# Kernel tuning notes

Hardware: AMD Instinct MI355X
Metric: run time of the kernel (lower is better)

Reference implementation:

```python
import jax, jax.numpy as jnp
import numpy as np

NUM_ENT = 100000   # entity vocabulary
NUM_EDGES = 200000 # KB pairs processed per hop (max_act)
D = 768            # BERT hidden size
NSTEP = 3          # num hops
QLEN = 32          # question length


def setup_inputs() -> dict:
    key = jax.random.key(0)
    ks = jax.random.split(key, 18)
    rn = lambda k, s, scale=1.0: jax.random.normal(k, s, dtype=jnp.float32) * scale
    W = 0.02  # weight init scale
    return {
        "q_emb": rn(ks[0], (1, D)),
        "q_word_h": rn(ks[1], (1, QLEN, D)),
        "desc_emb": rn(ks[2], (NUM_EDGES, D)),
        "step_w1": rn(ks[3], (NSTEP, D, D), W),
        "step_b1": rn(ks[4], (NSTEP, D), W),
        "step_w2": rn(ks[5], (NSTEP, D, D), W),
        "step_b2": rn(ks[6], (NSTEP, D), W),
        "rel_w1": rn(ks[7], (D, 256), W),
        "rel_b1": rn(ks[8], (256,), W),
        "rel_w2": rn(ks[9], (256,), W),
        "rel_b2": rn(ks[10], (1,), W),
        "hop_w1": rn(ks[11], (D, 256), W),
        "hop_b1": rn(ks[12], (256,), W),
        "hop_w2": rn(ks[13], (256, NSTEP), W),
        "hop_b2": rn(ks[14], (NSTEP,), W),
        "kb_pair": jax.random.randint(ks[15], (NUM_EDGES, 2), 0, NUM_ENT, dtype=jnp.int32),
        "topic_ent_idxs": jax.random.randint(ks[16], (4,), 0, NUM_ENT, dtype=jnp.int32),
    }


def reference(q_emb, q_word_h, desc_emb, step_w1, step_b1, step_w2, step_b2,
              rel_w1, rel_b1, rel_w2, rel_b2, hop_w1, hop_b1, hop_w2, hop_b2,
              kb_pair, topic_ent_idxs):
    gelu = lambda x: jax.nn.gelu(x, approximate=False)  # torch nn.GELU default
    # topic entity one-hot init (idx_to_one_hot)
    last_e = jnp.zeros((NUM_ENT,), jnp.float32).at[topic_ent_idxs].set(1.0)
    sub, obj = kb_pair[:, 0], kb_pair[:, 1]
    ent_probs = []
    for t in range(NSTEP):
        # step encoder: Linear -> GELU -> Linear
        cq = gelu(q_emb @ step_w1[t] + step_b1[t]) @ step_w2[t] + step_b2[t]  # [1,D]
        # attention over question words
        q_logits = jnp.einsum('bd,bld->bl', cq, q_word_h)                      # [1,L]
        q_dist = jax.nn.softmax(q_logits, axis=1)
        ctx = jnp.einsum('bl,bld->bd', q_dist, q_word_h) + cq                  # [1,D]
        # relation classifier over edge descriptions: Linear -> GELU -> Linear
        h = gelu((ctx * desc_emb) @ rel_w1 + rel_b1)                           # [E,256]
        d_prob = jax.nn.sigmoid(h @ rel_w2 + rel_b2)                           # [E]
        # follow: gather subject scores, scatter-add to objects
        obj_p = last_e[sub] * d_prob
        last_e = jax.ops.segment_sum(obj_p, obj, num_segments=NUM_ENT)
        # clamp-style renormalization (detached divisor)
        z = jax.lax.stop_gradient(jnp.where(last_e > 1.0, last_e, 1.0))
        last_e = last_e / z
        ent_probs.append(last_e)
    hop_res = jnp.stack(ent_probs, 0)                                          # [T,N]
    hop_attn = jax.nn.softmax(gelu(q_emb @ hop_w1 + hop_b1) @ hop_w2 + hop_b2, axis=1)  # [1,T]
    return (hop_attn @ hop_res)[0]                                             # [N]
```

## Files before the change

kernel.cpp:

```cpp
#include <hip/hip_runtime.h>
#include <math.h>

#define NUM_ENT 100000
#define NUM_EDGES 200000
#define DIM 768
#define BM 64
#define KSTEPS 24
#define NC 16
#define DCH 48

typedef float f32x4 __attribute__((ext_vector_type(4)));
typedef __bf16 bf16x8 __attribute__((ext_vector_type(8)));

#define WS_Y1    0
#define WS_CQ    2304
#define WS_HA    4704
#define WS_HOP1  4736
#define WS_CTX   4992
#define WS_B     7424
#define WS_DPROB 302336
#define WS_P1    302336
#define WS_P1H   339200
#define WS_P2    343296
#define WS_E     902336

__device__ __forceinline__ unsigned short f2bf(float f) {
    unsigned int x = __builtin_bit_cast(unsigned int, f);
    x = x + 0x7fffu + ((x >> 16) & 1u);
    return (unsigned short)(x >> 16);
}

__device__ __forceinline__ float gelu_f(float x) {
    float z = 0.70710678118654752f * x;
    float s = fabsf(z);
    float t = 1.f / (1.f + 0.3275911f * s);
    float p = t * (0.254829592f + t * (-0.284496736f + t * (1.421413741f +
              t * (-1.453152027f + t * 1.061405429f))));
    float e = __expf(-s * s);
    float erfa = copysignf(1.f - p * e, z);
    return 0.5f * x * (1.f + erfa);
}

__global__ void k1a(const float* __restrict__ q, const float* __restrict__ sw1,
                    const float* __restrict__ hw1, float* __restrict__ ws) {
    int b = blockIdx.x, tid = threadIdx.x;
    if (b < 48) {
        int t = b >> 4, c = b & 15;
        const float* w = sw1 + (size_t)t * DIM * DIM + (size_t)c * DCH * DIM;
        float a0 = 0.f, a1 = 0.f, a2 = 0.f;
        for (int d = 0; d < DCH; ++d) {
            float qv = q[c * DCH + d];
            const float* wr = w + (size_t)d * DIM;
            a0 += qv * wr[tid]; a1 += qv * wr[tid + 256]; a2 += qv * wr[tid + 512];
        }
        float* p = ws + WS_P1 + (size_t)b * DIM;
        p[tid] = a0; p[tid + 256] = a1; p[tid + 512] = a2;
    } else {
        int c = b - 48;
        const float* w = hw1 + (size_t)c * DCH * 256;
        float a0 = 0.f;
        for (int d = 0; d < DCH; ++d) a0 += q[c * DCH + d] * w[(size_t)d * 256 + tid];
        ws[WS_P1H + c * 256 + tid] = a0;
    }
}

__global__ void k1b(const float* __restrict__ sb1, const float* __restrict__ hb1,
                    float* __restrict__ ws) {
    int o = blockIdx.x * 256 + threadIdx.x;
    if (o < 2304) {
        int t = o / DIM, j = o % DIM;
        float s = sb1[o];
        for (int c = 0; c < NC; ++c) s += ws[WS_P1 + (size_t)(t * 16 + c) * DIM + j];
        ws[WS_Y1 + o] = gelu_f(s);
    } else if (o < 2560) {
        int j = o - 2304;
        float s = hb1[j];
        for (int c = 0; c < NC; ++c) s += ws[WS_P1H + c * 256 + j];
        ws[WS_HOP1 + j] = gelu_f(s);
    }
}

__global__ void k2a(const float* __restrict__ sw2, float* __restrict__ ws) {
    int b = blockIdx.x, tid = threadIdx.x;
    int t = b >> 4, c = b & 15;
    const float* w = sw2 + (size_t)t * DIM * DIM + (size_t)c * DCH * DIM;
    const float* y = ws + WS_Y1 + t * DIM + c * DCH;
    float a0 = 0.f, a1 = 0.f, a2 = 0.f;
    for (int d = 0; d < DCH; ++d) {
        float yv = y[d];
        const float* wr = w + (size_t)d * DIM;
        a0 += yv * wr[tid]; a1 += yv * wr[tid + 256]; a2 += yv * wr[tid + 512];
    }
    float* p = ws + WS_P2 + (size_t)b * DIM;
    p[tid] = a0; p[tid + 256] = a1; p[tid + 512] = a2;
}

__global__ void k2b(const float* __restrict__ sb2, float* __restrict__ ws) {
    int o = blockIdx.x * 256 + threadIdx.x;
    int t = o / DIM, j = o % DIM;
    float s = sb2[o];
    for (int c = 0; c < NC; ++c) s += ws[WS_P2 + (size_t)(t * 16 + c) * DIM + j];
    ws[WS_CQ + o] = s;
}

__global__ void k345(const float* __restrict__ qwh, const float* __restrict__ hw2,
                     const float* __restrict__ hb2, float* __restrict__ ws) {
    __shared__ float qlog[96];
    int tid = threadIdx.x;
    int w = tid >> 6, lane = tid & 63;
    for (int s = 0; s < 6; ++s) {
        int p = w * 6 + s;
        int t = p >> 5, l = p & 31;
        const float* c = ws + WS_CQ + t * DIM;
        const float* qw = qwh + l * DIM;
        float acc = 0.f;
        for (int i = lane; i < DIM; i += 64) acc += c[i] * qw[i];
        for (int m = 32; m; m >>= 1) acc += __shfl_xor(acc, m);
        if (lane == 0) qlog[p] = acc;
    }
    __syncthreads();
    if (tid < 64) {
        for (int t = 0; t < 3; ++t) {
            float v = (lane < 32) ? qlog[t * 32 + lane] : -1e30f;
            float mx = v;
            for (int m = 1; m < 32; m <<= 1) mx = fmaxf(mx, __shfl_xor(mx, m, 32));
            float e = (lane < 32) ? __expf(v - mx) : 0.f;
            float s = e;
            for (int m = 1; m < 32; m <<= 1) s += __shfl_xor(s, m, 32);
            if (lane < 32) qlog[t * 32 + lane] = e / s;
        }
        float lg = 0.f;
        if (lane < 3) {
            for (int s = 0; s < 256; ++s) lg += ws[WS_HOP1 + s] * hw2[s * 3 + lane];
            lg += hb2[lane];
        }
        float l0 = __shfl(lg, 0), l1 = __shfl(lg, 1), l2 = __shfl(lg, 2);
        if (lane == 0) {
            float mx = fmaxf(l0, fmaxf(l1, l2));
            float e0 = __expf(l0 - mx), e1 = __expf(l1 - mx), e2 = __expf(l2 - mx);
            float s = e0 + e1 + e2;
            ws[WS_HA + 0] = e0 / s; ws[WS_HA + 1] = e1 / s; ws[WS_HA + 2] = e2 / s;
        }
    }
    __syncthreads();
    for (int o = tid; o < 2304; o += 1024) {
        int t = o / DIM, d = o % DIM;
        float acc = ws[WS_CQ + o];
        const float* qd = qlog + t * 32;
        for (int l = 0; l < 32; ++l) acc += qd[l] * qwh[l * DIM + d];
        ws[WS_CTX + o] = acc;
    }
}

__global__ void k6_bmat(const float* __restrict__ rw1, float* __restrict__ ws) {
    int g = blockIdx.x * 256 + threadIdx.x;
    int lane = g & 63, f = g >> 6;
    int ks = f / 48, r = f % 48;
    int t = r >> 4, cf = r & 15;
    int k0 = ks * 32 + (lane >> 4) * 8;
    int col = cf * 16 + (lane & 15);
    const float* ctx = ws + WS_CTX + t * DIM;
    union { unsigned short u[8]; bf16x8 v; } pk;
    #pragma unroll
    for (int j = 0; j < 8; ++j) {
        float v = ctx[k0 + j] * rw1[(size_t)(k0 + j) * 256 + col];
        pk.u[j] = f2bf(v);
    }
    *(bf16x8*)((unsigned short*)(ws + WS_B) + (size_t)g * 8) = pk.v;
}

#define MFMA4(A, B0, B1, B2, B3, RF)                                               \
    acc[RF][0] = __builtin_amdgcn_mfma_f32_16x16x32_bf16(A, B0, acc[RF][0], 0,0,0); \
    acc[RF][1] = __builtin_amdgcn_mfma_f32_16x16x32_bf16(A, B1, acc[RF][1], 0,0,0); \
    acc[RF][2] = __builtin_amdgcn_mfma_f32_16x16x32_bf16(A, B2, acc[RF][2], 0,0,0); \
    acc[RF][3] = __builtin_amdgcn_mfma_f32_16x16x32_bf16(A, B3, acc[RF][3], 0,0,0);

#define MSTEP(KS, B0, B1, B2, B3) {                                                \
    const unsigned short* ab = ab0 + (size_t)(KS) * 2048;                          \
    bf16x8 a;                                                                      \
    a = *(const bf16x8*)(ab);          MFMA4(a, B0, B1, B2, B3, 0)                 \
    a = *(const bf16x8*)(ab + 512);    MFMA4(a, B0, B1, B2, B3, 1)                 \
    a = *(const bf16x8*)(ab + 1024);   MFMA4(a, B0, B1, B2, B3, 2)                 \
    a = *(const bf16x8*)(ab + 1536);   MFMA4(a, B0, B1, B2, B3, 3)                 \
}

#define LOADB(N0, N1, N2, N3, KS) {                                                \
    const unsigned short* p = bp0 + (size_t)(KS) * 24576;                          \
    N0 = *(const bf16x8*)(p);        N1 = *(const bf16x8*)(p + 512);               \
    N2 = *(const bf16x8*)(p + 1024); N3 = *(const bf16x8*)(p + 1536);              \
}

__global__ __launch_bounds__(768, 3)
void k7_gemm(const float* __restrict__ desc, const float* __restrict__ rb1,
             const float* __restrict__ rw2, const float* __restrict__ rb2,
             float* __restrict__ ws) {
    extern __shared__ char lds[];
    unsigned short* aLds = (unsigned short*)lds;
    float* part = (float*)(lds + 98304);

    const unsigned short* bmat = (const unsigned short*)(ws + WS_B);
    float* dprob = ws + WS_DPROB;
    int tid = threadIdx.x, blk = blockIdx.x;
    int wid = tid >> 6, lane = tid & 63;
    int t = wid >> 2, cg = wid & 3;
    int fbase = (t << 4) + (cg << 2);

    const unsigned short* bp0 = bmat + ((size_t)fbase << 9) + lane * 8;

    bf16x8 bA0, bA1, bA2, bA3, bB0, bB1, bB2, bB3;
    bf16x8 bC0, bC1, bC2, bC3, bD0, bD1, bD2, bD3;
    LOADB(bA0, bA1, bA2, bA3, 0)
    LOADB(bB0, bB1, bB2, bB3, 1)
    LOADB(bC0, bC1, bC2, bC3, 2)
    LOADB(bD0, bD1, bD2, bD3, 3)

    #pragma unroll
    for (int i = 0; i < 8; ++i) {
        int gf = i * 768 + tid;
        int l = gf & 63, f = gf >> 6;
        int ks = f >> 2, rf = f & 3;
        int row = rf * 16 + (l & 15);
        int kb = ks * 32 + (l >> 4) * 8;
        const float* src = desc + (size_t)(blk * BM + row) * DIM + kb;
        float4 v0 = *(const float4*)src;
        float4 v1 = *(const float4*)(src + 4);
        bf16x8 pk;
        pk[0] = (__bf16)v0.x; pk[1] = (__bf16)v0.y; pk[2] = (__bf16)v0.z; pk[3] = (__bf16)v0.w;
        pk[4] = (__bf16)v1.x; pk[5] = (__bf16)v1.y; pk[6] = (__bf16)v1.z; pk[7] = (__bf16)v1.w;
        *(bf16x8*)(aLds + (size_t)f * 512 + l * 8) = pk;
    }
    __syncthreads();

    f32x4 acc[4][4];
    #pragma unroll
    for (int rf = 0; rf < 4; ++rf)
        #pragma unroll
        for (int i = 0; i < 4; ++i) acc[rf][i] = f32x4{0.f, 0.f, 0.f, 0.f};

    const unsigned short* ab0 = aLds + lane * 8;

    #pragma unroll 1
    for (int it = 0; it < 6; ++it) {
        int ks = it * 4;
        MSTEP(ks,     bA0, bA1, bA2, bA3)
        if (it < 5) LOADB(bA0, bA1, bA2, bA3, ks + 4)
        MSTEP(ks + 1, bB0, bB1, bB2, bB3)
        if (it < 5) LOADB(bB0, bB1, bB2, bB3, ks + 5)
        MSTEP(ks + 2, bC0, bC1, bC2, bC3)
        if (it < 5) LOADB(bC0, bC1, bC2, bC3, ks + 6)
        MSTEP(ks + 3, bD0, bD1, bD2, bD3)
        if (it < 5) LOADB(bD0, bD1, bD2, bD3, ks + 7)
    }

    int col16 = lane & 15, quart = lane >> 4;
    float b1v[4], w2v[4];
    #pragma unroll
    for (int i = 0; i < 4; ++i) {
        int c = cg * 64 + i * 16 + col16;
        b1v[i] = rb1[c]; w2v[i] = rw2[c];
    }
    #pragma unroll
    for (int rf = 0; rf < 4; ++rf) {
        #pragma unroll
        for (int r = 0; r < 4; ++r) {
            float s = 0.f;
            #pragma unroll
            for (int i = 0; i < 4; ++i)
                s += gelu_f(acc[rf][i][r] + b1v[i]) * w2v[i];
            #pragma unroll
            for (int m = 1; m < 16; m <<= 1) s += __shfl_xor(s, m);
            if (col16 == 0) part[wid * 64 + rf * 16 + quart * 4 + r] = s;
        }
    }
    __syncthreads();
    if (tid < 192) {
        int tt = tid >> 6, row = tid & 63;
        float v = part[(tt * 4 + 0) * 64 + row] + part[(tt * 4 + 1) * 64 + row]
                + part[(tt * 4 + 2) * 64 + row] + part[(tt * 4 + 3) * 64 + row] + rb2[0];
        float p = 1.f / (1.f + __expf(-v));
        dprob[(size_t)tt * NUM_EDGES + blk * BM + row] = p;
    }
}

__global__ void kzero(float* __restrict__ ws) {
    int i = blockIdx.x * 256 + threadIdx.x;
    if (i < 3 * NUM_ENT) ws[WS_E + NUM_ENT + i] = 0.f;
}

__global__ void k9_scatter(const int* __restrict__ kb, const int* __restrict__ topics,
                           float* __restrict__ ws, int t) {
    int e = blockIdx.x * 256 + threadIdx.x;
    if (e >= NUM_EDGES) return;
    int sub = kb[2 * e], obj = kb[2 * e + 1];
    float g;
    if (t == 0) {
        g = (sub == topics[0] || sub == topics[1] || sub == topics[2] || sub == topics[3]) ? 1.f : 0.f;
    } else {
        float v = ws[WS_E + (size_t)t * NUM_ENT + sub];
        g = v / fmaxf(v, 1.f);
    }
    float p = g * ws[WS_DPROB + (size_t)t * NUM_EDGES + e];
    if (p != 0.f) atomicAdd(&ws[WS_E + (size_t)(t + 1) * NUM_ENT + obj], p);
}

__global__ void kout(const float* __restrict__ ws, float* __restrict__ out) {
    int i = blockIdx.x * 256 + threadIdx.x;
    if (i >= NUM_ENT) return;
    float v1 = ws[WS_E + 1 * NUM_ENT + i]; v1 /= fmaxf(v1, 1.f);
    float v2 = ws[WS_E + 2 * NUM_ENT + i]; v2 /= fmaxf(v2, 1.f);
    float v3 = ws[WS_E + 3 * NUM_ENT + i]; v3 /= fmaxf(v3, 1.f);
    out[i] = ws[WS_HA + 0] * v1 + ws[WS_HA + 1] * v2 + ws[WS_HA + 2] * v3;
}

extern "C" void kernel_launch(void* const* d_in, const int* in_sizes, int n_in,
                              void* d_out, int out_size, void* d_ws, size_t ws_size,
                              hipStream_t stream) {
    const float* q_emb   = (const float*)d_in[0];
    const float* qwh     = (const float*)d_in[1];
    const float* desc    = (const float*)d_in[2];
    const float* sw1     = (const float*)d_in[3];
    const float* sb1     = (const float*)d_in[4];
    const float* sw2     = (const float*)d_in[5];
    const float* sb2     = (const float*)d_in[6];
    const float* rw1     = (const float*)d_in[7];
    const float* rb1     = (const float*)d_in[8];
    const float* rw2     = (const float*)d_in[9];
    const float* rb2     = (const float*)d_in[10];
    const float* hw1     = (const float*)d_in[11];
    const float* hb1     = (const float*)d_in[12];
    const float* hw2     = (const float*)d_in[13];
    const float* hb2     = (const float*)d_in[14];
    const int*   kb      = (const int*)d_in[15];
    const int*   topics  = (const int*)d_in[16];
    float* ws  = (float*)d_ws;
    float* out = (float*)d_out;

    int nblk7 = NUM_EDGES / BM;

    kzero<<<(3 * NUM_ENT + 255) / 256, 256, 0, stream>>>(ws);
    k1a<<<64, 256, 0, stream>>>(q_emb, sw1, hw1, ws);
    k1b<<<10, 256, 0, stream>>>(sb1, hb1, ws);
    k2a<<<48, 256, 0, stream>>>(sw2, ws);
    k2b<<<9, 256, 0, stream>>>(sb2, ws);
    k345<<<1, 1024, 0, stream>>>(qwh, hw2, hb2, ws);
    k6_bmat<<<288, 256, 0, stream>>>(rw1, ws);
    k7_gemm<<<nblk7, 768, 101376, stream>>>(desc, rb1, rw2, rb2, ws);
    for (int t = 0; t < 3; ++t)
        k9_scatter<<<(NUM_EDGES + 255) / 256, 256, 0, stream>>>(kb, topics, ws, t);
    kout<<<(NUM_ENT + 255) / 256, 256, 0, stream>>>(ws, out);
}
```

Measured before the change: 475.0 us.

## Halve GEMM row tile and deepen B-fragment register pipeline in k7

```diff
diff --git a/kernel.cpp b/kernel.cpp
--- a/kernel.cpp
+++ b/kernel.cpp
@@ -4,12 +4,13 @@
 #define NUM_ENT 100000
 #define NUM_EDGES 200000
 #define DIM 768
-#define BM 64
+#define BM 32
 #define KSTEPS 24
 #define NC 16
 #define DCH 48
 
 typedef float f32x4 __attribute__((ext_vector_type(4)));
+typedef float f32x4e __attribute__((ext_vector_type(4)));
 typedef __bf16 bf16x8 __attribute__((ext_vector_type(8)));
 
 #define WS_Y1    0
@@ -169,34 +170,13 @@
     *(bf16x8*)((unsigned short*)(ws + WS_B) + (size_t)g * 8) = pk.v;
 }
 
-#define MFMA4(A, B0, B1, B2, B3, RF)                                               \
-    acc[RF][0] = __builtin_amdgcn_mfma_f32_16x16x32_bf16(A, B0, acc[RF][0], 0,0,0); \
-    acc[RF][1] = __builtin_amdgcn_mfma_f32_16x16x32_bf16(A, B1, acc[RF][1], 0,0,0); \
-    acc[RF][2] = __builtin_amdgcn_mfma_f32_16x16x32_bf16(A, B2, acc[RF][2], 0,0,0); \
-    acc[RF][3] = __builtin_amdgcn_mfma_f32_16x16x32_bf16(A, B3, acc[RF][3], 0,0,0);
-
-#define MSTEP(KS, B0, B1, B2, B3) {                                                \
-    const unsigned short* ab = ab0 + (size_t)(KS) * 2048;                          \
-    bf16x8 a;                                                                      \
-    a = *(const bf16x8*)(ab);          MFMA4(a, B0, B1, B2, B3, 0)                 \
-    a = *(const bf16x8*)(ab + 512);    MFMA4(a, B0, B1, B2, B3, 1)                 \
-    a = *(const bf16x8*)(ab + 1024);   MFMA4(a, B0, B1, B2, B3, 2)                 \
-    a = *(const bf16x8*)(ab + 1536);   MFMA4(a, B0, B1, B2, B3, 3)                 \
-}
-
-#define LOADB(N0, N1, N2, N3, KS) {                                                \
-    const unsigned short* p = bp0 + (size_t)(KS) * 24576;                          \
-    N0 = *(const bf16x8*)(p);        N1 = *(const bf16x8*)(p + 512);               \
-    N2 = *(const bf16x8*)(p + 1024); N3 = *(const bf16x8*)(p + 1536);              \
-}
-
 __global__ __launch_bounds__(768, 3)
 void k7_gemm(const float* __restrict__ desc, const float* __restrict__ rb1,
              const float* __restrict__ rw2, const float* __restrict__ rb2,
              float* __restrict__ ws) {
     extern __shared__ char lds[];
     unsigned short* aLds = (unsigned short*)lds;
-    float* part = (float*)(lds + 98304);
+    float* part = (float*)(lds + 49152);
 
     const unsigned short* bmat = (const unsigned short*)(ws + WS_B);
     float* dprob = ws + WS_DPROB;
@@ -207,23 +187,24 @@
 
     const unsigned short* bp0 = bmat + ((size_t)fbase << 9) + lane * 8;
 
-    bf16x8 bA0, bA1, bA2, bA3, bB0, bB1, bB2, bB3;
-    bf16x8 bC0, bC1, bC2, bC3, bD0, bD1, bD2, bD3;
-    LOADB(bA0, bA1, bA2, bA3, 0)
-    LOADB(bB0, bB1, bB2, bB3, 1)
-    LOADB(bC0, bC1, bC2, bC3, 2)
-    LOADB(bD0, bD1, bD2, bD3, 3)
-
-    #pragma unroll
-    for (int i = 0; i < 8; ++i) {
+    bf16x8 bset[6][4];
+    #pragma unroll
+    for (int s = 0; s < 6; ++s) {
+        const unsigned short* p = bp0 + (size_t)s * 24576;
+        #pragma unroll
+        for (int i = 0; i < 4; ++i) bset[s][i] = *(const bf16x8*)(p + i * 512);
+    }
+
+    #pragma unroll
+    for (int i = 0; i < 4; ++i) {
         int gf = i * 768 + tid;
         int l = gf & 63, f = gf >> 6;
-        int ks = f >> 2, rf = f & 3;
+        int ks = f >> 1, rf = f & 1;
         int row = rf * 16 + (l & 15);
         int kb = ks * 32 + (l >> 4) * 8;
         const float* src = desc + (size_t)(blk * BM + row) * DIM + kb;
-        float4 v0 = *(const float4*)src;
-        float4 v1 = *(const float4*)(src + 4);
+        f32x4e v0 = __builtin_nontemporal_load((const f32x4e*)src);
+        f32x4e v1 = __builtin_nontemporal_load((const f32x4e*)(src + 4));
         bf16x8 pk;
         pk[0] = (__bf16)v0.x; pk[1] = (__bf16)v0.y; pk[2] = (__bf16)v0.z; pk[3] = (__bf16)v0.w;
         pk[4] = (__bf16)v1.x; pk[5] = (__bf16)v1.y; pk[6] = (__bf16)v1.z; pk[7] = (__bf16)v1.w;
@@ -231,25 +212,39 @@
     }
     __syncthreads();
 
-    f32x4 acc[4][4];
-    #pragma unroll
-    for (int rf = 0; rf < 4; ++rf)
+    f32x4 acc[2][4];
+    #pragma unroll
+    for (int rf = 0; rf < 2; ++rf)
         #pragma unroll
         for (int i = 0; i < 4; ++i) acc[rf][i] = f32x4{0.f, 0.f, 0.f, 0.f};
 
     const unsigned short* ab0 = aLds + lane * 8;
 
-    #pragma unroll 1
-    for (int it = 0; it < 6; ++it) {
-        int ks = it * 4;
-        MSTEP(ks,     bA0, bA1, bA2, bA3)
-        if (it < 5) LOADB(bA0, bA1, bA2, bA3, ks + 4)
-        MSTEP(ks + 1, bB0, bB1, bB2, bB3)
-        if (it < 5) LOADB(bB0, bB1, bB2, bB3, ks + 5)
-        MSTEP(ks + 2, bC0, bC1, bC2, bC3)
-        if (it < 5) LOADB(bC0, bC1, bC2, bC3, ks + 6)
-        MSTEP(ks + 3, bD0, bD1, bD2, bD3)
-        if (it < 5) LOADB(bD0, bD1, bD2, bD3, ks + 7)
+    bf16x8 aa[2][2];
+    aa[0][0] = *(const bf16x8*)(ab0);
+    aa[0][1] = *(const bf16x8*)(ab0 + 512);
+
+    const unsigned short* bl = bp0 + 6 * 24576;
+
+    #pragma unroll
+    for (int ks = 0; ks < KSTEPS; ++ks) {
+        const int cs = ks % 6, cu = ks & 1, nx = cu ^ 1;
+        if (ks < KSTEPS - 1) {
+            aa[nx][0] = *(const bf16x8*)(ab0 + (ks + 1) * 1024);
+            aa[nx][1] = *(const bf16x8*)(ab0 + (ks + 1) * 1024 + 512);
+        }
+        #pragma unroll
+        for (int i = 0; i < 4; ++i)
+            acc[0][i] = __builtin_amdgcn_mfma_f32_16x16x32_bf16(aa[cu][0], bset[cs][i], acc[0][i], 0, 0, 0);
+        #pragma unroll
+        for (int i = 0; i < 4; ++i)
+            acc[1][i] = __builtin_amdgcn_mfma_f32_16x16x32_bf16(aa[cu][1], bset[cs][i], acc[1][i], 0, 0, 0);
+        if (ks < KSTEPS - 6) {
+            #pragma unroll
+            for (int i = 0; i < 4; ++i) bset[cs][i] = *(const bf16x8*)(bl + i * 512);
+            bl += 24576;
+        }
+        __builtin_amdgcn_sched_barrier(0);
     }
 
     int col16 = lane & 15, quart = lane >> 4;
@@ -260,7 +255,7 @@
         b1v[i] = rb1[c]; w2v[i] = rw2[c];
     }
     #pragma unroll
-    for (int rf = 0; rf < 4; ++rf) {
+    for (int rf = 0; rf < 2; ++rf) {
         #pragma unroll
         for (int r = 0; r < 4; ++r) {
             float s = 0.f;
@@ -269,14 +264,14 @@
                 s += gelu_f(acc[rf][i][r] + b1v[i]) * w2v[i];
             #pragma unroll
             for (int m = 1; m < 16; m <<= 1) s += __shfl_xor(s, m);
-            if (col16 == 0) part[wid * 64 + rf * 16 + quart * 4 + r] = s;
+            if (col16 == 0) part[wid * 32 + rf * 16 + quart * 4 + r] = s;
         }
     }
     __syncthreads();
-    if (tid < 192) {
-        int tt = tid >> 6, row = tid & 63;
-        float v = part[(tt * 4 + 0) * 64 + row] + part[(tt * 4 + 1) * 64 + row]
-                + part[(tt * 4 + 2) * 64 + row] + part[(tt * 4 + 3) * 64 + row] + rb2[0];
+    if (tid < 96) {
+        int tt = tid >> 5, row = tid & 31;
+        float v = part[(tt * 4 + 0) * 32 + row] + part[(tt * 4 + 1) * 32 + row]
+                + part[(tt * 4 + 2) * 32 + row] + part[(tt * 4 + 3) * 32 + row] + rb2[0];
         float p = 1.f / (1.f + __expf(-v));
         dprob[(size_t)tt * NUM_EDGES + blk * BM + row] = p;
     }
@@ -344,7 +339,7 @@
     k2b<<<9, 256, 0, stream>>>(sb2, ws);
     k345<<<1, 1024, 0, stream>>>(qwh, hw2, hb2, ws);
     k6_bmat<<<288, 256, 0, stream>>>(rw1, ws);
-    k7_gemm<<<nblk7, 768, 101376, stream>>>(desc, rb1, rw2, rb2, ws);
+    k7_gemm<<<nblk7, 768, 50688, stream>>>(desc, rb1, rw2, rb2, ws);
     for (int t = 0; t < 3; ++t)
         k9_scatter<<<(NUM_EDGES + 255) / 256, 256, 0, stream>>>(kb, topics, ws, t);
     kout<<<(NUM_ENT + 255) / 256, 256, 0, stream>>>(ws, out);
```

New measurement: 518.7 us. 1.09x slower.
